# Performance work log

Hardware: AMD Instinct MI355X
Metric: run time of the kernel (lower is better)

The kernel has to match this reference:

```python
import jax, jax.numpy as jnp
import numpy as np
from jax import lax

B, T, A = 64, 1024, 512
FILTERS, K = 32, 31
PAD = (K - 1) // 2


def setup_inputs() -> dict:
    key = jax.random.key(0)
    ks = jax.random.split(key, 12)
    return {
        "encoder_seq_proj": jax.random.normal(ks[0], (B, T, A), jnp.float32),
        "query": jax.random.normal(ks[1], (B, A), jnp.float32),
        "cumulative": jax.random.uniform(ks[2], (B, T), jnp.float32),
        "attention": jax.random.uniform(ks[3], (B, T), jnp.float32),
        "alpha": jax.random.uniform(ks[4], (B, T), jnp.float32),
        "conv_w": jax.random.normal(ks[5], (FILTERS, 2, K), jnp.float32) * 0.1,
        "L_w": jax.random.normal(ks[6], (A, FILTERS), jnp.float32) * 0.1,
        "L_b": jax.random.normal(ks[7], (A,), jnp.float32) * 0.1,
        "W_w": jax.random.normal(ks[8], (A, A), jnp.float32) * 0.05,
        "W_b": jax.random.normal(ks[9], (A,), jnp.float32) * 0.05,
        "v_w": jax.random.normal(ks[10], (1, A), jnp.float32) * 0.05,
        "t": 1,
        "phone_len": jax.random.randint(ks[11], (B,), 1, T + 1).astype(jnp.int64),
    }


def reference(encoder_seq_proj, query, cumulative, attention, alpha,
              conv_w, L_w, L_b, W_w, W_b, v_w, t, phone_len):
    # attention mask from phone lengths (set at init, reused each step)
    mask = (jnp.arange(T)[None, :] < phone_len[:, None]).astype(encoder_seq_proj.dtype)
    # processed query: [B, 1, A]
    pq = (query @ W_w.T + W_b)[:, None, :]
    # location features: stack cumulative + previous attention -> [B, 2, T]
    loc = jnp.stack([cumulative, attention], axis=1)
    conv_out = lax.conv_general_dilated(
        loc, conv_w, window_strides=(1,), padding=[(PAD, PAD)],
        dimension_numbers=("NCH", "OIH", "NCH"))  # [B, F, T]
    ploc = jnp.einsum("bft,af->bta", conv_out, L_w) + L_b  # [B, T, A]
    # additive energies -> [B, T]
    u = jnp.einsum("bta,a->bt", jnp.tanh(pq + encoder_seq_proj + ploc), v_w[0])
    s = jax.nn.sigmoid(u)
    scores = s / jnp.sum(s, axis=1, keepdims=True)
    att = scores * mask
    # forward-attention recursion (enable_forward_bias=True path)
    shift_alpha = jnp.pad(alpha[:, :-1], ((0, 0), (1, 0)))
    dual_alpha = jnp.pad(alpha[:, :-2], ((0, 0), (2, 0)))
    new_alpha = (shift_alpha + dual_alpha + alpha + 1e-7) * att
    new_alpha = new_alpha / jnp.sum(new_alpha, axis=-1, keepdims=True)
    return new_alpha[:, None, :]  # [B, 1, T]
```

## Files before the change

### kernel.cpp

```cpp
#include <hip/hip_runtime.h>

#define NB 64
#define NT 1024
#define NA 512
#define NF 32
#define KW 31
#define PADW 15
#define TC 64
#define CWN (2 * KW * NF)

typedef __fp16 half2v __attribute__((ext_vector_type(2)));

__device__ __forceinline__ float fast_tanh(float x) {
    float e = __builtin_amdgcn_exp2f(x * 2.885390081777927f);
    return 1.0f - 2.0f * __builtin_amdgcn_rcpf(1.0f + e);
}
__device__ __forceinline__ float fast_sigmoid(float u) {
    return __builtin_amdgcn_rcpf(1.0f + __builtin_amdgcn_exp2f(-u * 1.4426950408889634f));
}
__device__ __forceinline__ unsigned pkrtz(float a, float b) {
    half2v h = __builtin_amdgcn_cvt_pkrtz(a, b);
    return __builtin_bit_cast(unsigned, h);
}
__device__ __forceinline__ float fdot2u(unsigned cv, unsigned lw, float acc) {
#if __has_builtin(__builtin_amdgcn_fdot2)
    return __builtin_amdgcn_fdot2(__builtin_bit_cast(half2v, cv),
                                  __builtin_bit_cast(half2v, lw), acc, false);
#else
    half2v a = __builtin_bit_cast(half2v, cv), b = __builtin_bit_cast(half2v, lw);
    return acc + (float)a.x * (float)b.x + (float)a.y * (float)b.y;
#endif
}

__global__ __launch_bounds__(256) void lsa_pq(
    const float* __restrict__ query, const float* __restrict__ Ww,
    const float* __restrict__ Wb, const float* __restrict__ convw,
    float* __restrict__ pq, float* __restrict__ cwT)
{
    if (blockIdx.x == 0) {
        for (int i = threadIdx.x; i < NF * 2 * KW; i += 256) {
            int f = i / (2 * KW);
            int r = i - f * 2 * KW;
            int c = r / KW;
            int k = r - c * KW;
            cwT[(c * KW + k) * NF + f] = convw[i];
        }
    }
    __shared__ float qs[NA];
    int tid  = threadIdx.x;
    int lane = tid & 63;
    int wv   = tid >> 6;
    int b     = blockIdx.x >> 3;
    int chunk = blockIdx.x & 7;
    qs[tid]       = query[b * NA + tid];
    qs[tid + 256] = query[b * NA + tid + 256];
    __syncthreads();

    float4 q0 = *(const float4*)(qs + 8 * lane);
    float4 q1 = *(const float4*)(qs + 8 * lane + 4);
#pragma unroll 4
    for (int i = 0; i < 16; ++i) {
        int a = chunk * 64 + wv * 16 + i;
        const float4* wr = (const float4*)(Ww + (long)a * NA + 8 * lane);
        float4 w0 = wr[0], w1 = wr[1];
        float s = w0.x * q0.x + w0.y * q0.y + w0.z * q0.z + w0.w * q0.w
                + w1.x * q1.x + w1.y * q1.y + w1.z * q1.z + w1.w * q1.w;
#pragma unroll
        for (int m = 1; m <= 32; m <<= 1) s += __shfl_xor(s, m, 64);
        if (lane == 0) pq[b * NA + a] = s + Wb[a];
    }
}

__global__ __launch_bounds__(256, 4) void lsa_main(
    const float* __restrict__ enc, const float* __restrict__ cum,
    const float* __restrict__ att, const float* __restrict__ cwT,
    const float* __restrict__ Lw, const float* __restrict__ Lb,
    const float* __restrict__ vw, const float* __restrict__ pq,
    float* __restrict__ sout)
{
    __shared__ float cw_s[CWN];
    __shared__ float cum_s[TC + 30];
    __shared__ float att_s[TC + 30];
    __shared__ unsigned cvsh[TC][20];
    __shared__ float wred[4][TC + 2];

    int tid  = threadIdx.x;
    int lane = tid & 63;
    int wv   = tid >> 6;
    int b    = blockIdx.x >> 4;
    int t0   = (blockIdx.x & 15) * TC;

    {
        const float4* src = (const float4*)cwT;
        float4* dst = (float4*)cw_s;
        if (tid < 248) {
            dst[tid]       = src[tid];
            dst[tid + 248] = src[tid + 248];
        }
    }
    if (tid < TC + 30) {
        int t = t0 - PADW + tid;
        bool ok = (t >= 0) && (t < NT);
        cum_s[tid] = ok ? cum[b * NT + t] : 0.f;
        att_s[tid] = ok ? att[b * NT + t] : 0.f;
    }

    int a0 = 2 * tid;
    const float4* lp = (const float4*)(Lw + (long)a0 * NF);
    unsigned h0[16], h1[16];
#pragma unroll
    for (int i = 0; i < 8; ++i) {
        float4 wa = lp[i];
        float4 wb = lp[8 + i];
        h0[2 * i]     = pkrtz(wa.x, wa.y);
        h0[2 * i + 1] = pkrtz(wa.z, wa.w);
        h1[2 * i]     = pkrtz(wb.x, wb.y);
        h1[2 * i + 1] = pkrtz(wb.z, wb.w);
    }
    float c0 = pq[b * NA + a0]     + Lb[a0];
    float c1 = pq[b * NA + a0 + 1] + Lb[a0 + 1];
    float vx = vw[a0], vy = vw[a0 + 1];
    __syncthreads();

    {
        int tt  = lane;
        int fbu = wv * 8;
        float acc[8] = {0, 0, 0, 0, 0, 0, 0, 0};
#pragma unroll
        for (int k = 0; k < KW; ++k) {
            float x0 = cum_s[tt + k];
            float x1 = att_s[tt + k];
            const float4* A  = (const float4*)(cw_s + k * NF + fbu);
            const float4* Bv = (const float4*)(cw_s + (KW + k) * NF + fbu);
#pragma unroll
            for (int j = 0; j < 2; ++j) {
                float4 wa = A[j], wb = Bv[j];
                acc[4 * j + 0] = fmaf(x0, wa.x, fmaf(x1, wb.x, acc[4 * j + 0]));
                acc[4 * j + 1] = fmaf(x0, wa.y, fmaf(x1, wb.y, acc[4 * j + 1]));
                acc[4 * j + 2] = fmaf(x0, wa.z, fmaf(x1, wb.z, acc[4 * j + 2]));
                acc[4 * j + 3] = fmaf(x0, wa.w, fmaf(x1, wb.w, acc[4 * j + 3]));
            }
        }
        uint4 pk;
        pk.x = pkrtz(acc[0], acc[1]);
        pk.y = pkrtz(acc[2], acc[3]);
        pk.z = pkrtz(acc[4], acc[5]);
        pk.w = pkrtz(acc[6], acc[7]);
        *(uint4*)&cvsh[tt][wv * 4] = pk;
    }
    __syncthreads();

    const float* erow = enc + ((long)b * NT + t0) * NA + a0;
#pragma unroll 1
    for (int half = 0; half < 2; ++half) {
        float p32[32];
#pragma unroll
        for (int tt = 0; tt < 32; ++tt) {
            int gtt = half * 32 + tt;
            float2 e = *(const float2*)(erow + (long)gtt * NA);
            float x0[2] = {c0 + e.x, 0.f};
            float x1[2] = {c1 + e.y, 0.f};
#pragma unroll
            for (int q = 0; q < 4; ++q) {
                uint4 cv = *(const uint4*)&cvsh[gtt][4 * q];
                int p = q & 1;
                x0[p] = fdot2u(cv.x, h0[4 * q + 0], x0[p]);
                x0[p] = fdot2u(cv.y, h0[4 * q + 1], x0[p]);
                x0[p] = fdot2u(cv.z, h0[4 * q + 2], x0[p]);
                x0[p] = fdot2u(cv.w, h0[4 * q + 3], x0[p]);
                x1[p] = fdot2u(cv.x, h1[4 * q + 0], x1[p]);
                x1[p] = fdot2u(cv.y, h1[4 * q + 1], x1[p]);
                x1[p] = fdot2u(cv.z, h1[4 * q + 2], x1[p]);
                x1[p] = fdot2u(cv.w, h1[4 * q + 3], x1[p]);
            }
            p32[tt] = fast_tanh(x0[0] + x0[1]) * vx + fast_tanh(x1[0] + x1[1]) * vy;
        }

        {
            int len = 32;
#pragma unroll
            for (int m = 1; m <= 16; m <<= 1) {
                int hlen = len >> 1;
                bool up = (lane & m) != 0;
#pragma unroll
                for (int i = 0; i < 16; ++i) {
                    if (i < hlen) {
                        float send = up ? p32[i] : p32[i + hlen];
                        float keep = up ? p32[i + hlen] : p32[i];
                        p32[i] = keep + __shfl_xor(send, m, 64);
                    }
                }
                len = hlen;
            }
            float v = p32[0] + __shfl_xor(p32[0], 32, 64);
            int l = lane & 31;
            int tt = ((l & 1) << 4) | ((l & 2) << 2) | (l & 4) | ((l & 8) >> 2) | ((l & 16) >> 4);
            if (lane < 32) wred[wv][half * 32 + tt] = v;
        }
    }
    __syncthreads();
    if (tid < TC) {
        float u = wred[0][tid] + wred[1][tid] + wred[2][tid] + wred[3][tid];
        sout[b * NT + t0 + tid] = fast_sigmoid(u);
    }
}

__global__ __launch_bounds__(256) void lsa_norm(
    const float* __restrict__ alpha, const int* __restrict__ plen,
    float* __restrict__ out)
{
    __shared__ float red[4];
    int tid = threadIdx.x;
    int b = blockIdx.x;
    int pl = plen[b];
    float w[4];
    float psum = 0.f;
#pragma unroll
    for (int j = 0; j < 4; ++j) {
        int t = tid + 256 * j;
        float s   = out[b * NT + t];
        float al  = alpha[b * NT + t];
        float am1 = (t >= 1) ? alpha[b * NT + t - 1] : 0.f;
        float am2 = (t >= 2) ? alpha[b * NT + t - 2] : 0.f;
        float val = (t < pl) ? (al + am1 + am2 + 1e-7f) * s : 0.f;
        w[j] = val;
        psum += val;
    }
#pragma unroll
    for (int m = 32; m >= 1; m >>= 1) psum += __shfl_xor(psum, m, 64);
    int lane = tid & 63, wid = tid >> 6;
    if (lane == 0) red[wid] = psum;
    __syncthreads();
    float total = red[0] + red[1] + red[2] + red[3];
    float inv = 1.0f / total;
#pragma unroll
    for (int j = 0; j < 4; ++j) {
        int t = tid + 256 * j;
        out[b * NT + t] = w[j] * inv;
    }
}

extern "C" void kernel_launch(void* const* d_in, const int* in_sizes, int n_in,
                              void* d_out, int out_size, void* d_ws, size_t ws_size,
                              hipStream_t stream)
{
    const float* enc   = (const float*)d_in[0];
    const float* query = (const float*)d_in[1];
    const float* cum   = (const float*)d_in[2];
    const float* att   = (const float*)d_in[3];
    const float* alpha = (const float*)d_in[4];
    const float* convw = (const float*)d_in[5];
    const float* Lw    = (const float*)d_in[6];
    const float* Lb    = (const float*)d_in[7];
    const float* Ww    = (const float*)d_in[8];
    const float* Wb    = (const float*)d_in[9];
    const float* vw    = (const float*)d_in[10];
    const int*   plen  = (const int*)d_in[12];

    float* pq  = (float*)d_ws;
    float* cwT = (float*)d_ws + NB * NA;
    float* sout = (float*)d_out;

    lsa_pq  <<<NB * 8,         256, 0, stream>>>(query, Ww, Wb, convw, pq, cwT);
    lsa_main<<<NB * (NT / TC), 256, 0, stream>>>(enc, cum, att, cwT, Lw, Lb, vw, pq, sout);
    lsa_norm<<<NB,             256, 0, stream>>>(alpha, plen, sout);
}
```

Measured before the change: 56.77 us.

## Broadcast conv features via readlane from registers instead of LDS reads

Each lane now loads one row of the packed conv features from LDS into 16 registers. The inner loop broadcasts each value to the wavefront with readlane, which removes the repeated per-timestep LDS uint4 loads. The time loop is split into four passes of 16 timesteps, so fewer partial values stay live and the butterfly reduction gets shorter. The cost is extra scalar readlane instructions, more shuffle stages per timestep, and a padded LDS stride for the staging buffer.

```diff
diff --git a/kernel.cpp b/kernel.cpp
--- a/kernel.cpp
+++ b/kernel.cpp
@@ -8,6 +8,7 @@
 #define PADW 15
 #define TC 64
 #define CWN (2 * KW * NF)
+#define CVST 68
 
 typedef __fp16 half2v __attribute__((ext_vector_type(2)));
 
@@ -81,7 +82,7 @@
     __shared__ float cw_s[CWN];
     __shared__ float cum_s[TC + 30];
     __shared__ float att_s[TC + 30];
-    __shared__ unsigned cvsh[TC][20];
+    __shared__ unsigned cvs[TC * CVST];
     __shared__ float wred[4][TC + 2];
 
     int tid  = threadIdx.x;
@@ -146,56 +147,73 @@
         pk.y = pkrtz(acc[2], acc[3]);
         pk.z = pkrtz(acc[4], acc[5]);
         pk.w = pkrtz(acc[6], acc[7]);
-        *(uint4*)&cvsh[tt][wv * 4] = pk;
-    }
-    __syncthreads();
+        *(uint4*)&cvs[tt * CVST + wv * 4] = pk;
+    }
+    __syncthreads();
+
+    unsigned creg[16];
+    {
+        const uint4* row = (const uint4*)&cvs[lane * CVST];
+#pragma unroll
+        for (int r = 0; r < 4; ++r) {
+            uint4 v = row[r];
+            creg[4 * r + 0] = v.x;
+            creg[4 * r + 1] = v.y;
+            creg[4 * r + 2] = v.z;
+            creg[4 * r + 3] = v.w;
+        }
+    }
 
     const float* erow = enc + ((long)b * NT + t0) * NA + a0;
 #pragma unroll 1
-    for (int half = 0; half < 2; ++half) {
-        float p32[32];
-#pragma unroll
-        for (int tt = 0; tt < 32; ++tt) {
-            int gtt = half * 32 + tt;
+    for (int pass = 0; pass < 4; ++pass) {
+        float p[16];
+#pragma unroll
+        for (int tt = 0; tt < 16; ++tt) {
+            int gtt = pass * 16 + tt;
             float2 e = *(const float2*)(erow + (long)gtt * NA);
             float x0[2] = {c0 + e.x, 0.f};
             float x1[2] = {c1 + e.y, 0.f};
 #pragma unroll
             for (int q = 0; q < 4; ++q) {
-                uint4 cv = *(const uint4*)&cvsh[gtt][4 * q];
-                int p = q & 1;
-                x0[p] = fdot2u(cv.x, h0[4 * q + 0], x0[p]);
-                x0[p] = fdot2u(cv.y, h0[4 * q + 1], x0[p]);
-                x0[p] = fdot2u(cv.z, h0[4 * q + 2], x0[p]);
-                x0[p] = fdot2u(cv.w, h0[4 * q + 3], x0[p]);
-                x1[p] = fdot2u(cv.x, h1[4 * q + 0], x1[p]);
-                x1[p] = fdot2u(cv.y, h1[4 * q + 1], x1[p]);
-                x1[p] = fdot2u(cv.z, h1[4 * q + 2], x1[p]);
-                x1[p] = fdot2u(cv.w, h1[4 * q + 3], x1[p]);
+                unsigned cv0 = __builtin_amdgcn_readlane(creg[4 * q + 0], gtt);
+                unsigned cv1 = __builtin_amdgcn_readlane(creg[4 * q + 1], gtt);
+                unsigned cv2 = __builtin_amdgcn_readlane(creg[4 * q + 2], gtt);
+                unsigned cv3 = __builtin_amdgcn_readlane(creg[4 * q + 3], gtt);
+                int pp = q & 1;
+                x0[pp] = fdot2u(cv0, h0[4 * q + 0], x0[pp]);
+                x0[pp] = fdot2u(cv1, h0[4 * q + 1], x0[pp]);
+                x0[pp] = fdot2u(cv2, h0[4 * q + 2], x0[pp]);
+                x0[pp] = fdot2u(cv3, h0[4 * q + 3], x0[pp]);
+                x1[pp] = fdot2u(cv0, h1[4 * q + 0], x1[pp]);
+                x1[pp] = fdot2u(cv1, h1[4 * q + 1], x1[pp]);
+                x1[pp] = fdot2u(cv2, h1[4 * q + 2], x1[pp]);
+                x1[pp] = fdot2u(cv3, h1[4 * q + 3], x1[pp]);
             }
-            p32[tt] = fast_tanh(x0[0] + x0[1]) * vx + fast_tanh(x1[0] + x1[1]) * vy;
+            p[tt] = fast_tanh(x0[0] + x0[1]) * vx + fast_tanh(x1[0] + x1[1]) * vy;
         }
 
         {
-            int len = 32;
-#pragma unroll
-            for (int m = 1; m <= 16; m <<= 1) {
+            int len = 16;
+#pragma unroll
+            for (int m = 1; m <= 8; m <<= 1) {
                 int hlen = len >> 1;
                 bool up = (lane & m) != 0;
 #pragma unroll
-                for (int i = 0; i < 16; ++i) {
+                for (int i = 0; i < 8; ++i) {
                     if (i < hlen) {
-                        float send = up ? p32[i] : p32[i + hlen];
-                        float keep = up ? p32[i + hlen] : p32[i];
-                        p32[i] = keep + __shfl_xor(send, m, 64);
+                        float send = up ? p[i] : p[i + hlen];
+                        float keep = up ? p[i + hlen] : p[i];
+                        p[i] = keep + __shfl_xor(send, m, 64);
                     }
                 }
                 len = hlen;
             }
-            float v = p32[0] + __shfl_xor(p32[0], 32, 64);
-            int l = lane & 31;
-            int tt = ((l & 1) << 4) | ((l & 2) << 2) | (l & 4) | ((l & 8) >> 2) | ((l & 16) >> 4);
-            if (lane < 32) wred[wv][half * 32 + tt] = v;
+            float v = p[0] + __shfl_xor(p[0], 16, 64);
+            v = v + __shfl_xor(v, 32, 64);
+            int l4 = lane & 15;
+            int tt = ((l4 & 1) << 3) | ((l4 & 2) << 1) | ((l4 & 4) >> 1) | ((l4 & 8) >> 3);
+            if (lane < 16) wred[wv][pass * 16 + tt] = v;
         }
     }
     __syncthreads();
```

Result: slower. 69.29 us (+22.1%).

## Split location convolution into separate kernel writing fp16 features to global

Applied to the files above, without the earlier changes.

Moves the 31-tap location convolution out of the main attention kernel into a new kernel that computes 256 timesteps per block and writes packed fp16 conv features to a workspace buffer. The main kernel then reads those features from global memory instead of computing them into shared memory, dropping two barriers and most of its shared memory footprint. This costs an extra kernel launch and a global round trip of about 4 MB of features.

```diff
diff --git a/kernel.cpp b/kernel.cpp
--- a/kernel.cpp
+++ b/kernel.cpp
@@ -8,6 +8,7 @@
 #define PADW 15
 #define TC 64
 #define CWN (2 * KW * NF)
+#define CVG_OFF 34752L
 
 typedef __fp16 half2v __attribute__((ext_vector_type(2)));
 
@@ -71,24 +72,17 @@
     }
 }
 
-__global__ __launch_bounds__(256, 4) void lsa_main(
-    const float* __restrict__ enc, const float* __restrict__ cum,
-    const float* __restrict__ att, const float* __restrict__ cwT,
-    const float* __restrict__ Lw, const float* __restrict__ Lb,
-    const float* __restrict__ vw, const float* __restrict__ pq,
-    float* __restrict__ sout)
+__global__ __launch_bounds__(256) void lsa_conv(
+    const float* __restrict__ cum, const float* __restrict__ att,
+    const float* __restrict__ cwT, unsigned* __restrict__ cvG)
 {
     __shared__ float cw_s[CWN];
-    __shared__ float cum_s[TC + 30];
-    __shared__ float att_s[TC + 30];
-    __shared__ unsigned cvsh[TC][20];
-    __shared__ float wred[4][TC + 2];
-
+    __shared__ float cum_s[256 + 30], att_s[256 + 30];
     int tid  = threadIdx.x;
     int lane = tid & 63;
     int wv   = tid >> 6;
-    int b    = blockIdx.x >> 4;
-    int t0   = (blockIdx.x & 15) * TC;
+    int b    = blockIdx.x >> 2;
+    int t0   = (blockIdx.x & 3) * 256;
 
     {
         const float4* src = (const float4*)cwT;
@@ -98,12 +92,56 @@
             dst[tid + 248] = src[tid + 248];
         }
     }
-    if (tid < TC + 30) {
-        int t = t0 - PADW + tid;
+    for (int i = tid; i < 256 + 30; i += 256) {
+        int t = t0 - PADW + i;
         bool ok = (t >= 0) && (t < NT);
-        cum_s[tid] = ok ? cum[b * NT + t] : 0.f;
-        att_s[tid] = ok ? att[b * NT + t] : 0.f;
-    }
+        cum_s[i] = ok ? cum[b * NT + t] : 0.f;
+        att_s[i] = ok ? att[b * NT + t] : 0.f;
+    }
+    __syncthreads();
+
+    int fbu = wv * 8;
+#pragma unroll 1
+    for (int sc = 0; sc < 4; ++sc) {
+        int tt = sc * 64 + lane;
+        float acc[8] = {0, 0, 0, 0, 0, 0, 0, 0};
+#pragma unroll
+        for (int k = 0; k < KW; ++k) {
+            float x0 = cum_s[tt + k];
+            float x1 = att_s[tt + k];
+            const float4* A  = (const float4*)(cw_s + k * NF + fbu);
+            const float4* Bv = (const float4*)(cw_s + (KW + k) * NF + fbu);
+#pragma unroll
+            for (int j = 0; j < 2; ++j) {
+                float4 wa = A[j], wb = Bv[j];
+                acc[4 * j + 0] = fmaf(x0, wa.x, fmaf(x1, wb.x, acc[4 * j + 0]));
+                acc[4 * j + 1] = fmaf(x0, wa.y, fmaf(x1, wb.y, acc[4 * j + 1]));
+                acc[4 * j + 2] = fmaf(x0, wa.z, fmaf(x1, wb.z, acc[4 * j + 2]));
+                acc[4 * j + 3] = fmaf(x0, wa.w, fmaf(x1, wb.w, acc[4 * j + 3]));
+            }
+        }
+        uint4 pk;
+        pk.x = pkrtz(acc[0], acc[1]);
+        pk.y = pkrtz(acc[2], acc[3]);
+        pk.z = pkrtz(acc[4], acc[5]);
+        pk.w = pkrtz(acc[6], acc[7]);
+        *(uint4*)&cvG[((long)(b * NT + t0 + tt)) * 16 + wv * 4] = pk;
+    }
+}
+
+__global__ __launch_bounds__(256, 4) void lsa_main(
+    const float* __restrict__ enc, const unsigned* __restrict__ cvG,
+    const float* __restrict__ Lw, const float* __restrict__ Lb,
+    const float* __restrict__ vw, const float* __restrict__ pq,
+    float* __restrict__ sout)
+{
+    __shared__ float wred[4][TC + 2];
+
+    int tid  = threadIdx.x;
+    int lane = tid & 63;
+    int wv   = tid >> 6;
+    int b    = blockIdx.x >> 4;
+    int t0   = (blockIdx.x & 15) * TC;
 
     int a0 = 2 * tid;
     const float4* lp = (const float4*)(Lw + (long)a0 * NF);
@@ -120,59 +158,41 @@
     float c0 = pq[b * NA + a0]     + Lb[a0];
     float c1 = pq[b * NA + a0 + 1] + Lb[a0 + 1];
     float vx = vw[a0], vy = vw[a0 + 1];
-    __syncthreads();
-
-    {
-        int tt  = lane;
-        int fbu = wv * 8;
-        float acc[8] = {0, 0, 0, 0, 0, 0, 0, 0};
-#pragma unroll
-        for (int k = 0; k < KW; ++k) {
-            float x0 = cum_s[tt + k];
-            float x1 = att_s[tt + k];
-            const float4* A  = (const float4*)(cw_s + k * NF + fbu);
-            const float4* Bv = (const float4*)(cw_s + (KW + k) * NF + fbu);
-#pragma unroll
-            for (int j = 0; j < 2; ++j) {
-                float4 wa = A[j], wb = Bv[j];
-                acc[4 * j + 0] = fmaf(x0, wa.x, fmaf(x1, wb.x, acc[4 * j + 0]));
-                acc[4 * j + 1] = fmaf(x0, wa.y, fmaf(x1, wb.y, acc[4 * j + 1]));
-                acc[4 * j + 2] = fmaf(x0, wa.z, fmaf(x1, wb.z, acc[4 * j + 2]));
-                acc[4 * j + 3] = fmaf(x0, wa.w, fmaf(x1, wb.w, acc[4 * j + 3]));
-            }
-        }
-        uint4 pk;
-        pk.x = pkrtz(acc[0], acc[1]);
-        pk.y = pkrtz(acc[2], acc[3]);
-        pk.z = pkrtz(acc[4], acc[5]);
-        pk.w = pkrtz(acc[6], acc[7]);
-        *(uint4*)&cvsh[tt][wv * 4] = pk;
-    }
-    __syncthreads();
-
+
+    const unsigned* cvrow = cvG + ((long)b * NT + t0) * 16;
     const float* erow = enc + ((long)b * NT + t0) * NA + a0;
+
+#define Q4(cv, hb)                                  \
+    {                                               \
+        x0[pp] = fdot2u(cv.x, h0[hb + 0], x0[pp]);  \
+        x0[pp] = fdot2u(cv.y, h0[hb + 1], x0[pp]);  \
+        x0[pp] = fdot2u(cv.z, h0[hb + 2], x0[pp]);  \
+        x0[pp] = fdot2u(cv.w, h0[hb + 3], x0[pp]);  \
+        x1[pp] = fdot2u(cv.x, h1[hb + 0], x1[pp]);  \
+        x1[pp] = fdot2u(cv.y, h1[hb + 1], x1[pp]);  \
+        x1[pp] = fdot2u(cv.z, h1[hb + 2], x1[pp]);  \
+        x1[pp] = fdot2u(cv.w, h1[hb + 3], x1[pp]);  \
+    }
+
 #pragma unroll 1
     for (int half = 0; half < 2; ++half) {
         float p32[32];
 #pragma unroll
         for (int tt = 0; tt < 32; ++tt) {
             int gtt = half * 32 + tt;
+            const uint4* cr = (const uint4*)(cvrow + (long)gtt * 16);
+            uint4 ca = cr[0], cb = cr[1], cc = cr[2], cd = cr[3];
             float2 e = *(const float2*)(erow + (long)gtt * NA);
             float x0[2] = {c0 + e.x, 0.f};
             float x1[2] = {c1 + e.y, 0.f};
-#pragma unroll
-            for (int q = 0; q < 4; ++q) {
-                uint4 cv = *(const uint4*)&cvsh[gtt][4 * q];
-                int p = q & 1;
-                x0[p] = fdot2u(cv.x, h0[4 * q + 0], x0[p]);
-                x0[p] = fdot2u(cv.y, h0[4 * q + 1], x0[p]);
-                x0[p] = fdot2u(cv.z, h0[4 * q + 2], x0[p]);
-                x0[p] = fdot2u(cv.w, h0[4 * q + 3], x0[p]);
-                x1[p] = fdot2u(cv.x, h1[4 * q + 0], x1[p]);
-                x1[p] = fdot2u(cv.y, h1[4 * q + 1], x1[p]);
-                x1[p] = fdot2u(cv.z, h1[4 * q + 2], x1[p]);
-                x1[p] = fdot2u(cv.w, h1[4 * q + 3], x1[p]);
-            }
+            int pp = 0;
+            Q4(ca, 0);
+            pp = 1;
+            Q4(cb, 4);
+            pp = 0;
+            Q4(cc, 8);
+            pp = 1;
+            Q4(cd, 12);
             p32[tt] = fast_tanh(x0[0] + x0[1]) * vx + fast_tanh(x1[0] + x1[1]) * vy;
         }
 
@@ -198,6 +218,7 @@
             if (lane < 32) wred[wv][half * 32 + tt] = v;
         }
     }
+#undef Q4
     __syncthreads();
     if (tid < TC) {
         float u = wred[0][tid] + wred[1][tid] + wred[2][tid] + wred[3][tid];
@@ -257,11 +278,13 @@
     const float* vw    = (const float*)d_in[10];
     const int*   plen  = (const int*)d_in[12];
 
-    float* pq  = (float*)d_ws;
-    float* cwT = (float*)d_ws + NB * NA;
-    float* sout = (float*)d_out;
+    float*    pq  = (float*)d_ws;
+    float*    cwT = (float*)d_ws + NB * NA;
+    unsigned* cvG = (unsigned*)d_ws + CVG_OFF;
+    float*    sout = (float*)d_out;
 
     lsa_pq  <<<NB * 8,         256, 0, stream>>>(query, Ww, Wb, convw, pq, cwT);
-    lsa_main<<<NB * (NT / TC), 256, 0, stream>>>(enc, cum, att, cwT, Lw, Lb, vw, pq, sout);
+    lsa_conv<<<NB * 4,         256, 0, stream>>>(cum, att, cwT, cvG);
+    lsa_main<<<NB * (NT / TC), 256, 0, stream>>>(enc, cvG, Lw, Lb, vw, pq, sout);
     lsa_norm<<<NB,             256, 0, stream>>>(alpha, plen, sout);
 }
```

Measured after the change: 76.40 us. +34.6%, slower.

## Remap main kernel threads to four attention columns over half the time tile

Applied to the files above, without the earlier changes.

Each thread now handles four consecutive A columns (float4 encoder loads) for 32 of the 64 timesteps, instead of two columns for all 64. Two waves cover one time half and are combined through shared memory. This widens global loads and shortens the cross-lane transpose reduction to eight values per group. In exchange it holds twice as many packed L_w weights in registers (64 values), which may lower occupancy under the 256,4 launch bound.

```diff
diff --git a/kernel.cpp b/kernel.cpp
--- a/kernel.cpp
+++ b/kernel.cpp
@@ -82,7 +82,7 @@
     __shared__ float cum_s[TC + 30];
     __shared__ float att_s[TC + 30];
     __shared__ unsigned cvsh[TC][20];
-    __shared__ float wred[4][TC + 2];
+    __shared__ float wred[4][34];
 
     int tid  = threadIdx.x;
     int lane = tid & 63;
@@ -105,21 +105,22 @@
         att_s[tid] = ok ? att[b * NT + t] : 0.f;
     }
 
-    int a0 = 2 * tid;
-    const float4* lp = (const float4*)(Lw + (long)a0 * NF);
-    unsigned h0[16], h1[16];
-#pragma unroll
-    for (int i = 0; i < 8; ++i) {
-        float4 wa = lp[i];
-        float4 wb = lp[8 + i];
-        h0[2 * i]     = pkrtz(wa.x, wa.y);
-        h0[2 * i + 1] = pkrtz(wa.z, wa.w);
-        h1[2 * i]     = pkrtz(wb.x, wb.y);
-        h1[2 * i + 1] = pkrtz(wb.z, wb.w);
-    }
-    float c0 = pq[b * NA + a0]     + Lb[a0];
-    float c1 = pq[b * NA + a0 + 1] + Lb[a0 + 1];
-    float vx = vw[a0], vy = vw[a0 + 1];
+    int a0  = (tid & 127) * 4;
+    int tth = tid >> 7;
+    unsigned h[4][16];
+    float c4[4], v4[4];
+#pragma unroll
+    for (int ai = 0; ai < 4; ++ai) {
+        const float4* lp = (const float4*)(Lw + (long)(a0 + ai) * NF);
+#pragma unroll
+        for (int i = 0; i < 8; ++i) {
+            float4 w = lp[i];
+            h[ai][2 * i]     = pkrtz(w.x, w.y);
+            h[ai][2 * i + 1] = pkrtz(w.z, w.w);
+        }
+        c4[ai] = pq[b * NA + a0 + ai] + Lb[a0 + ai];
+        v4[ai] = vw[a0 + ai];
+    }
     __syncthreads();
 
     {
@@ -150,57 +151,71 @@
     }
     __syncthreads();
 
-    const float* erow = enc + ((long)b * NT + t0) * NA + a0;
+#define DOA(ai, ecomp)                                                  \
+    {                                                                   \
+        float y0 = 0.f, y1 = 0.f;                                       \
+        y0 = fdot2u(cva.x, h[ai][0],  y0); y1 = fdot2u(cva.y, h[ai][1],  y1); \
+        y0 = fdot2u(cva.z, h[ai][2],  y0); y1 = fdot2u(cva.w, h[ai][3],  y1); \
+        y0 = fdot2u(cvb.x, h[ai][4],  y0); y1 = fdot2u(cvb.y, h[ai][5],  y1); \
+        y0 = fdot2u(cvb.z, h[ai][6],  y0); y1 = fdot2u(cvb.w, h[ai][7],  y1); \
+        y0 = fdot2u(cvc.x, h[ai][8],  y0); y1 = fdot2u(cvc.y, h[ai][9],  y1); \
+        y0 = fdot2u(cvc.z, h[ai][10], y0); y1 = fdot2u(cvc.w, h[ai][11], y1); \
+        y0 = fdot2u(cvd.x, h[ai][12], y0); y1 = fdot2u(cvd.y, h[ai][13], y1); \
+        y0 = fdot2u(cvd.z, h[ai][14], y0); y1 = fdot2u(cvd.w, h[ai][15], y1); \
+        s = fmaf(fast_tanh(y0 + y1 + c4[ai] + (ecomp)), v4[ai], s);     \
+    }
+
+    const float* erow = enc + ((long)b * NT + t0 + tth * 32) * NA + a0;
 #pragma unroll 1
-    for (int half = 0; half < 2; ++half) {
-        float p32[32];
-#pragma unroll
-        for (int tt = 0; tt < 32; ++tt) {
-            int gtt = half * 32 + tt;
-            float2 e = *(const float2*)(erow + (long)gtt * NA);
-            float x0[2] = {c0 + e.x, 0.f};
-            float x1[2] = {c1 + e.y, 0.f};
-#pragma unroll
-            for (int q = 0; q < 4; ++q) {
-                uint4 cv = *(const uint4*)&cvsh[gtt][4 * q];
-                int p = q & 1;
-                x0[p] = fdot2u(cv.x, h0[4 * q + 0], x0[p]);
-                x0[p] = fdot2u(cv.y, h0[4 * q + 1], x0[p]);
-                x0[p] = fdot2u(cv.z, h0[4 * q + 2], x0[p]);
-                x0[p] = fdot2u(cv.w, h0[4 * q + 3], x0[p]);
-                x1[p] = fdot2u(cv.x, h1[4 * q + 0], x1[p]);
-                x1[p] = fdot2u(cv.y, h1[4 * q + 1], x1[p]);
-                x1[p] = fdot2u(cv.z, h1[4 * q + 2], x1[p]);
-                x1[p] = fdot2u(cv.w, h1[4 * q + 3], x1[p]);
-            }
-            p32[tt] = fast_tanh(x0[0] + x0[1]) * vx + fast_tanh(x1[0] + x1[1]) * vy;
+    for (int g = 0; g < 4; ++g) {
+        float p[8];
+#pragma unroll
+        for (int j = 0; j < 8; ++j) {
+            int tt  = g * 8 + j;
+            int gtt = tth * 32 + tt;
+            float4 e = *(const float4*)(erow + (long)tt * NA);
+            uint4 cva = *(const uint4*)&cvsh[gtt][0];
+            uint4 cvb = *(const uint4*)&cvsh[gtt][4];
+            uint4 cvc = *(const uint4*)&cvsh[gtt][8];
+            uint4 cvd = *(const uint4*)&cvsh[gtt][12];
+            float s = 0.f;
+            DOA(0, e.x)
+            DOA(1, e.y)
+            DOA(2, e.z)
+            DOA(3, e.w)
+            p[j] = s;
         }
 
         {
-            int len = 32;
-#pragma unroll
-            for (int m = 1; m <= 16; m <<= 1) {
+            int len = 8;
+#pragma unroll
+            for (int m = 1; m <= 4; m <<= 1) {
                 int hlen = len >> 1;
                 bool up = (lane & m) != 0;
 #pragma unroll
-                for (int i = 0; i < 16; ++i) {
+                for (int i = 0; i < 4; ++i) {
                     if (i < hlen) {
-                        float send = up ? p32[i] : p32[i + hlen];
-                        float keep = up ? p32[i + hlen] : p32[i];
-                        p32[i] = keep + __shfl_xor(send, m, 64);
+                        float send = up ? p[i] : p[i + hlen];
+                        float keep = up ? p[i + hlen] : p[i];
+                        p[i] = keep + __shfl_xor(send, m, 64);
                     }
                 }
                 len = hlen;
             }
-            float v = p32[0] + __shfl_xor(p32[0], 32, 64);
-            int l = lane & 31;
-            int tt = ((l & 1) << 4) | ((l & 2) << 2) | (l & 4) | ((l & 8) >> 2) | ((l & 16) >> 4);
-            if (lane < 32) wred[wv][half * 32 + tt] = v;
-        }
-    }
+            float v = p[0];
+            v += __shfl_xor(v, 8, 64);
+            v += __shfl_xor(v, 16, 64);
+            v += __shfl_xor(v, 32, 64);
+            int l3 = lane & 7;
+            int tt = ((l3 & 1) << 2) | (l3 & 2) | ((l3 & 4) >> 2);
+            if (lane < 8) wred[wv][g * 8 + tt] = v;
+        }
+    }
+#undef DOA
     __syncthreads();
     if (tid < TC) {
-        float u = wred[0][tid] + wred[1][tid] + wred[2][tid] + wred[3][tid];
+        float u = (tid < 32) ? (wred[0][tid] + wred[1][tid])
+                             : (wred[2][tid - 32] + wred[3][tid - 32]);
         sout[b * NT + t0 + tid] = fast_sigmoid(u);
     }
 }
```

Result: slower. 65.17 us (+14.8%).
